# Optimization experiments

Hardware: AMD Instinct MI355X
Metric: run time of the kernel (lower is better)

The kernel has to match this reference:

```python
import jax, jax.numpy as jnp
import numpy as np

B, N, C, H = 4, 2048, 1024, 16
HD = C // H
SCALE = HD ** -0.5


def setup_inputs() -> dict:
    key = jax.random.key(0)
    k1, k2, k3, k4 = jax.random.split(key, 4)
    x = jax.random.normal(k1, (B, N, C), dtype=jnp.float32)
    # torch nn.Linear weights: [out, in]
    w_qkv = jax.random.normal(k2, (3 * C, C), dtype=jnp.float32) * (C ** -0.5)
    w_proj = jax.random.normal(k3, (C, C), dtype=jnp.float32) * (C ** -0.5)
    b_proj = jax.random.normal(k4, (C,), dtype=jnp.float32) * 0.01
    return {"x": x, "w_qkv": w_qkv, "w_proj": w_proj, "b_proj": b_proj}


def reference(x, w_qkv, w_proj, b_proj):
    Bx, Nx, Cx = x.shape
    # qkv projection: [B,N,3C] -> [3,B,H,N,HD]
    qkv = jnp.einsum('bnc,dc->bnd', x, w_qkv)
    qkv = qkv.reshape(Bx, Nx, 3, H, HD).transpose(2, 0, 3, 1, 4)
    q, k, v = qkv[0], qkv[1], qkv[2]
    attn = jnp.einsum('bhqd,bhkd->bhqk', q, k) * SCALE
    attn = jax.nn.softmax(attn, axis=-1)
    # dropout p=0.0 (eval/identity)
    out = jnp.einsum('bhqk,bhkd->bhqd', attn, v)
    out = out.transpose(0, 2, 1, 3).reshape(Bx, Nx, Cx)
    return jnp.einsum('bnc,dc->bnd', out, w_proj) + b_proj
```

## Files before the change

kernel.cpp:

```cpp
#include <hip/hip_runtime.h>


typedef float f32x2 __attribute__((ext_vector_type(2)));
typedef float f32x4 __attribute__((ext_vector_type(4)));
typedef float f32x16 __attribute__((ext_vector_type(16)));
typedef __bf16 bf16x8 __attribute__((ext_vector_type(8)));
typedef __bf16 bf16x4 __attribute__((ext_vector_type(4)));
typedef __bf16 bf16x2 __attribute__((ext_vector_type(2)));
typedef unsigned int u32;
typedef unsigned int u32x2 __attribute__((ext_vector_type(2)));

__device__ __forceinline__ void async16(const void* g, void* l) {
  __builtin_amdgcn_global_load_lds((const __attribute__((address_space(1))) unsigned int*)g,
                                   (__attribute__((address_space(3))) unsigned int*)l, 16, 0, 0);
}
__device__ __forceinline__ u32 cvtpk_bf16(float lo, float hi) {
  u32 r;
  asm("v_cvt_pk_bf16_f32 %0, %1, %2" : "=v"(r) : "v"(lo), "v"(hi));
  return r;
}
__device__ __forceinline__ void swap32(u32& a, u32& b) {
  asm volatile("v_permlane32_swap_b32 %0, %1" : "+v"(a), "+v"(b));
}
__device__ __forceinline__ float xmax64(float x) { return fmaxf(x, __shfl_xor(x, 32, 64)); }
__device__ __forceinline__ float xsum64(float x) { return x + __shfl_xor(x, 32, 64); }
__device__ __forceinline__ float exp2v(float x) { return __builtin_amdgcn_exp2f(x); }
__device__ __forceinline__ f32x2 pkmax(f32x2 a, f32x2 b) {
  return f32x2{ fmaxf(a.x, b.x), fmaxf(a.y, b.y) };
}

__global__ __launch_bounds__(256) void cast_to_bf16(const float* __restrict__ x,
                                                    const float* __restrict__ wq,
                                                    const float* __restrict__ wp,
                                                    __bf16* __restrict__ xo,
                                                    __bf16* __restrict__ wqo,
                                                    __bf16* __restrict__ wpo) {
  long i = (long)blockIdx.x * 256 + threadIdx.x;
  const float* s; __bf16* d; long j;
  if (i < 2097152L)      { s = x;  d = xo;  j = i; }
  else if (i < 2883584L) { s = wq; d = wqo; j = i - 2097152L; }
  else                   { s = wp; d = wpo; j = i - 2883584L; }
  float4 v = ((const float4*)s)[j];
  bf16x4 o = { (__bf16)v.x, (__bf16)v.y, (__bf16)v.z, (__bf16)v.w };
  ((bf16x4*)d)[j] = o;
}

template <int EPI>
__global__ __launch_bounds__(256) void gemm_bt(const __bf16* __restrict__ A,
                                               const __bf16* __restrict__ Bw,
                                               __bf16* __restrict__ Oq,
                                               float* __restrict__ Of,
                                               const float* __restrict__ bias) {
  const int tid = threadIdx.x;
  const int lane = tid & 63, w = tid >> 6;
  const int arow = lane & 15, agrp = lane >> 4;
  const int wm = w >> 1, wn = w & 1;
  const int bm = blockIdx.x, bn = blockIdx.y;
  __shared__ __bf16 As[128 * 32];
  __shared__ __bf16 Bs[128 * 32];
  f32x4 acc[4][4] = {};

  const int c0 = tid, c1 = tid + 256;
  const __bf16* Ag0 = A + ((size_t)(bm * 128 + (c0 >> 2)) << 10) + (c0 & 3) * 8;
  const __bf16* Ag1 = A + ((size_t)(bm * 128 + (c1 >> 2)) << 10) + (c1 & 3) * 8;
  const __bf16* Bg0 = Bw + ((size_t)(bn * 128 + (c0 >> 2)) << 10) + (c0 & 3) * 8;
  const __bf16* Bg1 = Bw + ((size_t)(bn * 128 + (c1 >> 2)) << 10) + (c1 & 3) * 8;

  for (int kt = 0; kt < 1024; kt += 32) {
    async16(Ag0 + kt, &As[c0 * 8]);
    async16(Ag1 + kt, &As[c1 * 8]);
    async16(Bg0 + kt, &Bs[c0 * 8]);
    async16(Bg1 + kt, &Bs[c1 * 8]);
    __syncthreads();
    bf16x8 af[4], bfr[4];
#pragma unroll
    for (int mi = 0; mi < 4; ++mi)
      af[mi] = *(const bf16x8*)&As[(wm * 64 + mi * 16 + arow) * 32 + agrp * 8];
#pragma unroll
    for (int ni = 0; ni < 4; ++ni)
      bfr[ni] = *(const bf16x8*)&Bs[(wn * 64 + ni * 16 + arow) * 32 + agrp * 8];
#pragma unroll
    for (int mi = 0; mi < 4; ++mi)
#pragma unroll
      for (int ni = 0; ni < 4; ++ni)
        acc[mi][ni] = __builtin_amdgcn_mfma_f32_16x16x32_bf16(af[mi], bfr[ni], acc[mi][ni], 0, 0, 0);
    __syncthreads();
  }

  const int rowb = bm * 128 + wm * 64 + agrp * 4;
  const int colb = bn * 128 + wn * 64 + arow;
  if (EPI == 0) {
#pragma unroll
    for (int mi = 0; mi < 4; ++mi) {
      const int row = rowb + mi * 16;
      const int bidx = row >> 11;
#pragma unroll
      for (int ni = 0; ni < 4; ++ni) {
        f32x4 v = acc[mi][ni];
        const int col = colb + ni * 16;
        const int which = col >> 10;
        const int h = (col >> 6) & 15;
        const int hd = col & 63;
        const float s = (which == 0) ? 0.18033688011112042f : 1.0f;
        __bf16* dst = Oq + ((size_t)which * 64 + bidx * 16 + h) * (size_t)(2048 * 64) + hd;
#pragma unroll
        for (int i = 0; i < 4; ++i)
          dst[(size_t)((row + i) & 2047) * 64] = (__bf16)(v[i] * s);
      }
    }
  } else {
#pragma unroll
    for (int mi = 0; mi < 4; ++mi) {
      const int row = rowb + mi * 16;
#pragma unroll
      for (int ni = 0; ni < 4; ++ni) {
        const int col = colb + ni * 16;
        const float bv = bias[col];
        f32x4 v = acc[mi][ni];
#pragma unroll
        for (int i = 0; i < 4; ++i)
          Of[(size_t)(row + i) * 1024 + col] = v[i] + bv;
      }
    }
  }
}

__global__ __launch_bounds__(256) void mhsa_attn(const __bf16* __restrict__ QKV,
                                                 __bf16* __restrict__ Out) {
  const int tid = threadIdx.x;
  const int lane = tid & 63, w = tid >> 6;
  const int blk = blockIdx.x;
  const int bh = blk & 63, qt = blk >> 6;
  const int lq = lane & 31, hi = lane >> 5;
  const int l7 = lane & 7;

  const size_t bhoff = (size_t)bh * (2048 * 64);
  const __bf16* Qp = QKV + bhoff;
  const __bf16* Kp = QKV + (size_t)(64 * 2048 * 64) + bhoff;
  const __bf16* Vp = QKV + (size_t)(128 * 2048 * 64) + bhoff;

  __shared__ char smem[16384];
  char* KsB = smem;
  char* VTB = smem + 8192;

  const int q0 = qt * 128 + w * 32;

  bf16x8 qf[4];
#pragma unroll
  for (int s = 0; s < 4; ++s)
    qf[s] = *(const bf16x8*)&Qp[(size_t)(q0 + lq) * 64 + s * 16 + hi * 8];

  f32x16 Oacc0 = 0.f, Oacc1 = 0.f;
  float m_run = -1e30f, l_run = 0.f;

  const int kr0 = tid >> 3, kc8 = tid & 7;
  const int kr1 = kr0 + 32;
  const int c8v = tid >> 5, k0v = (tid & 31) * 2;

  for (int kt = 0; kt < 2048; kt += 64) {
    bf16x8 kv0 = *(const bf16x8*)&Kp[(size_t)(kt + kr0) * 64 + kc8 * 8];
    bf16x8 kv1 = *(const bf16x8*)&Kp[(size_t)(kt + kr1) * 64 + kc8 * 8];
    bf16x8 v0 = *(const bf16x8*)&Vp[(size_t)(kt + k0v) * 64 + c8v * 8];
    bf16x8 v1 = *(const bf16x8*)&Vp[(size_t)(kt + k0v + 1) * 64 + c8v * 8];
    *(bf16x8*)(KsB + ((kr0 * 128 + kc8 * 16) ^ ((kr0 & 7) << 4))) = kv0;
    *(bf16x8*)(KsB + ((kr1 * 128 + kc8 * 16) ^ ((kr1 & 7) << 4))) = kv1;
#pragma unroll
    for (int j = 0; j < 8; ++j) {
      const int d = c8v * 8 + j;
      bf16x2 pr = { v0[j], v1[j] };
      *(bf16x2*)(VTB + ((d * 128 + k0v * 2) ^ ((d & 7) << 4))) = pr;
    }
    __syncthreads();

    f32x16 st0 = 0.f, st1 = 0.f;
    __builtin_amdgcn_s_setprio(1);
#pragma unroll
    for (int s = 0; s < 4; ++s) {
      bf16x8 kf = *(const bf16x8*)(KsB + lq * 128 + ((s * 32 + hi * 16) ^ (l7 << 4)));
      st0 = __builtin_amdgcn_mfma_f32_32x32x16_bf16(kf, qf[s], st0, 0, 0, 0);
    }
#pragma unroll
    for (int s = 0; s < 4; ++s) {
      bf16x8 kf = *(const bf16x8*)(KsB + (32 + lq) * 128 + ((s * 32 + hi * 16) ^ (l7 << 4)));
      st1 = __builtin_amdgcn_mfma_f32_32x32x16_bf16(kf, qf[s], st1, 0, 0, 0);
    }
    __builtin_amdgcn_s_setprio(0);

    f32x2 m2 = f32x2{ st0[0], st0[1] };
#pragma unroll
    for (int r = 1; r < 8; ++r) m2 = pkmax(m2, f32x2{ st0[2 * r], st0[2 * r + 1] });
#pragma unroll
    for (int r = 0; r < 8; ++r) m2 = pkmax(m2, f32x2{ st1[2 * r], st1[2 * r + 1] });
    float mx = xmax64(fmaxf(m2.x, m2.y));

    if (!__all(mx - m_run <= 8.f)) {
      const float mnew = fmaxf(m_run, mx);
      const float fs = exp2v(m_run - mnew);
      m_run = mnew;
      l_run *= fs;
#pragma unroll
      for (int r = 0; r < 16; ++r) { Oacc0[r] *= fs; Oacc1[r] *= fs; }
    }

    const float mb = m_run;
#pragma unroll
    for (int r = 0; r < 16; ++r) st0[r] = exp2v(st0[r] - mb);
#pragma unroll
    for (int r = 0; r < 16; ++r) st1[r] = exp2v(st1[r] - mb);
    f32x2 s2 = f32x2{ st0[0], st0[1] };
#pragma unroll
    for (int r = 1; r < 8; ++r) s2 += f32x2{ st0[2 * r], st0[2 * r + 1] };
#pragma unroll
    for (int r = 0; r < 8; ++r) s2 += f32x2{ st1[2 * r], st1[2 * r + 1] };
    l_run += xsum64(s2.x + s2.y);

    bf16x8 pa[4];
#pragma unroll
    for (int kb = 0; kb < 2; ++kb) {
      const f32x16& st = kb ? st1 : st0;
#pragma unroll
      for (int s16 = 0; s16 < 2; ++s16) {
        u32 A0 = cvtpk_bf16(st[8 * s16 + 0], st[8 * s16 + 1]);
        u32 B0 = cvtpk_bf16(st[8 * s16 + 4], st[8 * s16 + 5]);
        swap32(A0, B0);
        u32 A1 = cvtpk_bf16(st[8 * s16 + 2], st[8 * s16 + 3]);
        u32 B1 = cvtpk_bf16(st[8 * s16 + 6], st[8 * s16 + 7]);
        swap32(A1, B1);
        union { u32 wv[4]; bf16x8 v; } uu;
        uu.wv[0] = A0; uu.wv[1] = A1; uu.wv[2] = B0; uu.wv[3] = B1;
        pa[kb * 2 + s16] = uu.v;
      }
    }

    __builtin_amdgcn_s_setprio(1);
#pragma unroll
    for (int ks = 0; ks < 4; ++ks) {
      bf16x8 vf = *(const bf16x8*)(VTB + lq * 128 + ((ks * 32 + hi * 16) ^ (l7 << 4)));
      Oacc0 = __builtin_amdgcn_mfma_f32_32x32x16_bf16(vf, pa[ks], Oacc0, 0, 0, 0);
    }
#pragma unroll
    for (int ks = 0; ks < 4; ++ks) {
      bf16x8 vf = *(const bf16x8*)(VTB + (32 + lq) * 128 + ((ks * 32 + hi * 16) ^ (l7 << 4)));
      Oacc1 = __builtin_amdgcn_mfma_f32_32x32x16_bf16(vf, pa[ks], Oacc1, 0, 0, 0);
    }
    __builtin_amdgcn_s_setprio(0);
    __syncthreads();
  }

  const float inv = 1.0f / l_run;
  const int b = bh >> 4, h = bh & 15;
  __bf16* orow = Out + ((size_t)(b * 2048 + q0 + lq)) * 1024 + h * 64;
#pragma unroll
  for (int db = 0; db < 2; ++db) {
    const f32x16& O = db ? Oacc1 : Oacc0;
#pragma unroll
    for (int rg = 0; rg < 4; ++rg) {
      u32 plo = cvtpk_bf16(O[rg * 4 + 0] * inv, O[rg * 4 + 1] * inv);
      u32 phi = cvtpk_bf16(O[rg * 4 + 2] * inv, O[rg * 4 + 3] * inv);
      u32x2 pk = { plo, phi };
      *(u32x2*)&orow[db * 32 + rg * 8 + hi * 4] = pk;
    }
  }
}

extern "C" void kernel_launch(void* const* d_in, const int* in_sizes, int n_in,
                              void* d_out, int out_size, void* d_ws, size_t ws_size,
                              hipStream_t stream) {
  const float* x  = (const float*)d_in[0];
  const float* wq = (const float*)d_in[1];
  const float* wp = (const float*)d_in[2];
  const float* bp = (const float*)d_in[3];
  char* ws = (char*)d_ws;

  __bf16* xo   = (__bf16*)(ws);
  __bf16* wqo  = (__bf16*)(ws + 16777216);
  __bf16* wpo  = (__bf16*)(ws + 23068672);
  __bf16* qkv  = (__bf16*)(ws + 25165824);
  __bf16* aout = xo;
  float* y = (float*)d_out;

  cast_to_bf16<<<12288, 256, 0, stream>>>(x, wq, wp, xo, wqo, wpo);
  gemm_bt<0><<<dim3(64, 24), 256, 0, stream>>>(xo, wqo, qkv, nullptr, nullptr);
  mhsa_attn<<<1024, 256, 0, stream>>>(qkv, aout);
  gemm_bt<1><<<dim3(64, 8), 256, 0, stream>>>(aout, wpo, nullptr, y, bp);
}
```

Measured before the change: 215.9 us.

## Double-buffer K/V tiles in LDS and prefetch next tile into registers

The attention loop now uses two LDS buffers for the K and transposed V tiles. The next tile's global loads are issued into registers before the current tile's QK^T, softmax and PV MFMAs, and written to the alternate buffer afterwards. This hides global load latency behind compute and removes one barrier per iteration. In exchange, LDS per block doubles to 32 KB and the prefetched values raise register pressure, which may reduce occupancy.

```diff
diff --git a/kernel.cpp b/kernel.cpp
--- a/kernel.cpp
+++ b/kernel.cpp
@@ -139,9 +139,7 @@
   const __bf16* Kp = QKV + (size_t)(64 * 2048 * 64) + bhoff;
   const __bf16* Vp = QKV + (size_t)(128 * 2048 * 64) + bhoff;
 
-  __shared__ char smem[16384];
-  char* KsB = smem;
-  char* VTB = smem + 8192;
+  __shared__ char smem[32768];
 
   const int q0 = qt * 128 + w * 32;
 
@@ -156,32 +154,53 @@
   const int kr0 = tid >> 3, kc8 = tid & 7;
   const int kr1 = kr0 + 32;
   const int c8v = tid >> 5, k0v = (tid & 31) * 2;
-
-  for (int kt = 0; kt < 2048; kt += 64) {
-    bf16x8 kv0 = *(const bf16x8*)&Kp[(size_t)(kt + kr0) * 64 + kc8 * 8];
-    bf16x8 kv1 = *(const bf16x8*)&Kp[(size_t)(kt + kr1) * 64 + kc8 * 8];
-    bf16x8 v0 = *(const bf16x8*)&Vp[(size_t)(kt + k0v) * 64 + c8v * 8];
-    bf16x8 v1 = *(const bf16x8*)&Vp[(size_t)(kt + k0v + 1) * 64 + c8v * 8];
-    *(bf16x8*)(KsB + ((kr0 * 128 + kc8 * 16) ^ ((kr0 & 7) << 4))) = kv0;
-    *(bf16x8*)(KsB + ((kr1 * 128 + kc8 * 16) ^ ((kr1 & 7) << 4))) = kv1;
+  const int koff0 = (kr0 * 128 + kc8 * 16) ^ ((kr0 & 7) << 4);
+  const int koff1 = (kr1 * 128 + kc8 * 16) ^ ((kr1 & 7) << 4);
+
+  {
+    bf16x8 kv0 = *(const bf16x8*)&Kp[(size_t)kr0 * 64 + kc8 * 8];
+    bf16x8 kv1 = *(const bf16x8*)&Kp[(size_t)kr1 * 64 + kc8 * 8];
+    bf16x8 v0 = *(const bf16x8*)&Vp[(size_t)k0v * 64 + c8v * 8];
+    bf16x8 v1 = *(const bf16x8*)&Vp[(size_t)(k0v + 1) * 64 + c8v * 8];
+    char* Kb = smem;
+    char* Vb = smem + 8192;
+    *(bf16x8*)(Kb + koff0) = kv0;
+    *(bf16x8*)(Kb + koff1) = kv1;
 #pragma unroll
     for (int j = 0; j < 8; ++j) {
       const int d = c8v * 8 + j;
       bf16x2 pr = { v0[j], v1[j] };
-      *(bf16x2*)(VTB + ((d * 128 + k0v * 2) ^ ((d & 7) << 4))) = pr;
-    }
-    __syncthreads();
+      *(bf16x2*)(Vb + ((d * 128 + k0v * 2) ^ ((d & 7) << 4))) = pr;
+    }
+  }
+  __syncthreads();
+
+  for (int t = 0; t < 32; ++t) {
+    char* Kc = smem + (t & 1) * 16384;
+    char* Vc = Kc + 8192;
+    char* Kn = smem + ((t & 1) ^ 1) * 16384;
+    char* Vn = Kn + 8192;
+
+    bf16x8 kv0n, kv1n, v0n, v1n;
+    const bool pf = (t < 31);
+    if (pf) {
+      const int ktn = (t + 1) * 64;
+      kv0n = *(const bf16x8*)&Kp[(size_t)(ktn + kr0) * 64 + kc8 * 8];
+      kv1n = *(const bf16x8*)&Kp[(size_t)(ktn + kr1) * 64 + kc8 * 8];
+      v0n = *(const bf16x8*)&Vp[(size_t)(ktn + k0v) * 64 + c8v * 8];
+      v1n = *(const bf16x8*)&Vp[(size_t)(ktn + k0v + 1) * 64 + c8v * 8];
+    }
 
     f32x16 st0 = 0.f, st1 = 0.f;
     __builtin_amdgcn_s_setprio(1);
 #pragma unroll
     for (int s = 0; s < 4; ++s) {
-      bf16x8 kf = *(const bf16x8*)(KsB + lq * 128 + ((s * 32 + hi * 16) ^ (l7 << 4)));
+      bf16x8 kf = *(const bf16x8*)(Kc + lq * 128 + ((s * 32 + hi * 16) ^ (l7 << 4)));
       st0 = __builtin_amdgcn_mfma_f32_32x32x16_bf16(kf, qf[s], st0, 0, 0, 0);
     }
 #pragma unroll
     for (int s = 0; s < 4; ++s) {
-      bf16x8 kf = *(const bf16x8*)(KsB + (32 + lq) * 128 + ((s * 32 + hi * 16) ^ (l7 << 4)));
+      bf16x8 kf = *(const bf16x8*)(Kc + (32 + lq) * 128 + ((s * 32 + hi * 16) ^ (l7 << 4)));
       st1 = __builtin_amdgcn_mfma_f32_32x32x16_bf16(kf, qf[s], st1, 0, 0, 0);
     }
     __builtin_amdgcn_s_setprio(0);
@@ -235,15 +254,26 @@
     __builtin_amdgcn_s_setprio(1);
 #pragma unroll
     for (int ks = 0; ks < 4; ++ks) {
-      bf16x8 vf = *(const bf16x8*)(VTB + lq * 128 + ((ks * 32 + hi * 16) ^ (l7 << 4)));
+      bf16x8 vf = *(const bf16x8*)(Vc + lq * 128 + ((ks * 32 + hi * 16) ^ (l7 << 4)));
       Oacc0 = __builtin_amdgcn_mfma_f32_32x32x16_bf16(vf, pa[ks], Oacc0, 0, 0, 0);
     }
 #pragma unroll
     for (int ks = 0; ks < 4; ++ks) {
-      bf16x8 vf = *(const bf16x8*)(VTB + (32 + lq) * 128 + ((ks * 32 + hi * 16) ^ (l7 << 4)));
+      bf16x8 vf = *(const bf16x8*)(Vc + (32 + lq) * 128 + ((ks * 32 + hi * 16) ^ (l7 << 4)));
       Oacc1 = __builtin_amdgcn_mfma_f32_32x32x16_bf16(vf, pa[ks], Oacc1, 0, 0, 0);
     }
     __builtin_amdgcn_s_setprio(0);
+
+    if (pf) {
+      *(bf16x8*)(Kn + koff0) = kv0n;
+      *(bf16x8*)(Kn + koff1) = kv1n;
+#pragma unroll
+      for (int j = 0; j < 8; ++j) {
+        const int d = c8v * 8 + j;
+        bf16x2 pr = { v0n[j], v1n[j] };
+        *(bf16x2*)(Vn + ((d * 128 + k0v * 2) ^ ((d & 7) << 4))) = pr;
+      }
+    }
     __syncthreads();
   }
 
```

Result: faster. 202.4 us (-6.3%).
